# Kernel tuning notes

Hardware: AMD Instinct MI355X
Metric: run time of the kernel (lower is better)

The kernel has to match this reference:

```python
import jax, jax.numpy as jnp
import numpy as np

EPS_BN = 1e-5
EPS_W = 1e-8


def setup_inputs() -> dict:
    key = jax.random.key(0)
    ks = jax.random.split(key, 6)
    B, N, S, D1, D2 = 8, 8192, 2048, 128, 256
    Cin = D1 + D2  # 384
    return {
        "points_position": jax.random.normal(ks[0], (B, 3, N), jnp.float32),
        "sampled_points_position": jax.random.normal(ks[1], (B, 3, S), jnp.float32),
        "skip_points_feature": jax.random.normal(ks[2], (B, D1, N), jnp.float32),
        "sampled_points_feature": jax.random.normal(ks[3], (B, D2, S), jnp.float32),
        "W1": jax.random.normal(ks[4], (256, Cin), jnp.float32) * 0.05,
        "b1": jnp.zeros((256,), jnp.float32),
        "g1": jnp.ones((256,), jnp.float32),
        "beta1": jnp.zeros((256,), jnp.float32),
        "W2": jax.random.normal(ks[5], (128, 256), jnp.float32) * 0.05,
        "b2": jnp.zeros((128,), jnp.float32),
        "g2": jnp.ones((128,), jnp.float32),
        "beta2": jnp.zeros((128,), jnp.float32),
    }


def _bn_relu(x, g, b):
    # train-mode BatchNorm1d over (batch, points) per channel, x: [B,N,C]
    mean = jnp.mean(x, axis=(0, 1), keepdims=True)
    var = jnp.mean(jnp.square(x - mean), axis=(0, 1), keepdims=True)  # biased var
    return jax.nn.relu((x - mean) * jax.lax.rsqrt(var + EPS_BN) * g + b)


def reference(points_position, sampled_points_position, skip_points_feature,
              sampled_points_feature, W1, b1, g1, beta1, W2, b2, g2, beta2):
    pos = points_position.transpose(0, 2, 1)            # [B,N,3]
    spos = sampled_points_position.transpose(0, 2, 1)   # [B,S,3]
    sfeat = sampled_points_feature.transpose(0, 2, 1)   # [B,S,D2]

    # squared pairwise distance [B,N,S]
    d = (jnp.sum(pos * pos, axis=-1, keepdims=True)
         - 2.0 * jnp.einsum("bnc,bsc->bns", pos, spos)
         + jnp.sum(spos * spos, axis=-1)[:, None, :])

    # 3 nearest neighbors (smallest distances)
    neg_d3, idx = jax.lax.top_k(-d, 3)                  # [B,N,3]
    d3 = -neg_d3
    w = 1.0 / (d3 + EPS_W)
    w = w / jnp.sum(w, axis=-1, keepdims=True)          # [B,N,3]

    gathered = jax.vmap(lambda f, i: f[i])(sfeat, idx)  # [B,N,3,D2]
    interp = jnp.einsum("bnk,bnkd->bnd", w, gathered)   # [B,N,D2]

    feat = jnp.concatenate([skip_points_feature.transpose(0, 2, 1), interp], axis=-1)  # [B,N,D1+D2]

    h = _bn_relu(jnp.einsum("bnc,oc->bno", feat, W1) + b1, g1, beta1)  # [B,N,256]
    h = _bn_relu(jnp.einsum("bnc,oc->bno", h, W2) + b2, g2, beta2)     # [B,N,128]
    return h.transpose(0, 2, 1)                          # [B,128,N]
```

## Files before the change

### kernel.cpp

```cpp
#include <hip/hip_runtime.h>

constexpr int BATCH = 8;
constexpr int NPT   = 8192;
constexpr int NSMP  = 2048;
constexpr int D1C   = 128;
constexpr int D2C   = 256;
constexpr int CIN   = 384;
constexpr int C1    = 256;
constexpr int C2    = 128;
constexpr int BN_TOTAL = BATCH * NPT;

constexpr int WM = 128, WN = 64, WK = 32;
constexpr int NRB = BN_TOTAL / WM;

typedef __bf16 bf16x8 __attribute__((ext_vector_type(8)));
typedef short  s16x8  __attribute__((ext_vector_type(8)));
typedef float  f32x4  __attribute__((ext_vector_type(4)));

__device__ __forceinline__ unsigned short f2bf(float x) {
  unsigned u = __builtin_bit_cast(unsigned, x);
  u += 0x7fffu + ((u >> 16) & 1u);
  return (unsigned short)(u >> 16);
}
__device__ __forceinline__ float bf2f(unsigned short h) {
  return __builtin_bit_cast(float, (unsigned)h << 16);
}

__device__ __forceinline__ void gld_lds16(const void* g, void* l) {
  __builtin_amdgcn_global_load_lds(
      (const __attribute__((address_space(1))) void*)g,
      (__attribute__((address_space(3))) void*)l, 16, 0, 0);
}

__global__ void transpose_k(const float* __restrict__ in, float* __restrict__ out,
                            int rows, int cols, long inBatch, long outBatch) {
  __shared__ float tile[32][33];
  const float* inb = in + (size_t)blockIdx.z * inBatch;
  float* outb = out + (size_t)blockIdx.z * outBatch;
  int c0 = blockIdx.x * 32;
  int r0 = blockIdx.y * 32;
  int tx = threadIdx.x, ty = threadIdx.y;
#pragma unroll
  for (int i = 0; i < 32; i += 8) {
    int r = r0 + ty + i;
    tile[ty + i][tx] = inb[(size_t)r * cols + c0 + tx];
  }
  __syncthreads();
#pragma unroll
  for (int i = 0; i < 32; i += 8) {
    int c = c0 + ty + i;
    outb[(size_t)c * rows + r0 + tx] = tile[tx][ty + i];
  }
}

__global__ void skip_to_featB(const float* __restrict__ skip,
                              unsigned short* __restrict__ featB) {
  __shared__ float tile[32][33];
  int b = blockIdx.z;
  int n0 = blockIdx.x * 32;
  int d0 = blockIdx.y * 32;
  int tx = threadIdx.x, ty = threadIdx.y;
#pragma unroll
  for (int i = 0; i < 32; i += 8) {
    tile[ty + i][tx] = skip[((size_t)b * D1C + d0 + ty + i) * NPT + n0 + tx];
  }
  __syncthreads();
#pragma unroll
  for (int i = 0; i < 32; i += 8) {
    int n = n0 + ty + i;
    featB[((size_t)b * NPT + n) * CIN + d0 + tx] = f2bf(tile[tx][ty + i]);
  }
}

__global__ void wprep(const float* __restrict__ W, unsigned short* __restrict__ Wh,
                      int total) {
  int i = blockIdx.x * 256 + threadIdx.x;
  if (i >= total) return;
  Wh[i] = f2bf(W[i]);
}

__global__ void pack_spos(const float* __restrict__ spos, float* __restrict__ sposI) {
  int g = blockIdx.x * 256 + threadIdx.x;
  int b = g >> 11, s = g & (NSMP - 1);
  const float* sp = spos + (size_t)b * 3 * NSMP;
  sposI[(size_t)g * 3 + 0] = sp[s];
  sposI[(size_t)g * 3 + 1] = sp[NSMP + s];
  sposI[(size_t)g * 3 + 2] = sp[2 * NSMP + s];
}

constexpr int SEG = NSMP / 4;

__global__ __launch_bounds__(256) void knn_kernel(
    const float* __restrict__ pos,
    const float* __restrict__ sposI,
    int* __restrict__ idx_out,
    float* __restrict__ wgt_out,
    int* __restrict__ flag_list,
    int* __restrict__ flag_count) {
  __shared__ float qs[3 * NSMP];
  __shared__ float mk[4][4][64];

  int tid = threadIdx.x;
  int wave = tid >> 6, lane = tid & 63;
  int blk = blockIdx.x;
  int b = blk >> 7;
  int n = ((blk & 127) << 6) + lane;

  const float4* src = (const float4*)(sposI + (size_t)b * 3 * NSMP);
  float4* dst = (float4*)qs;
  for (int t = tid; t < 3 * NSMP / 4; t += 256) dst[t] = src[t];
  __syncthreads();

  const float* pb = pos + (size_t)b * 3 * NPT;
  float px = pb[n], py = pb[NPT + n], pz = pb[2 * NPT + n];

  const float INF = __builtin_inff();
  float k0 = INF, k1 = INF, k2 = INF, k3 = INF;

  const float4* q4 = (const float4*)qs;
  int s0 = wave * SEG;

#define KNN_STEP(QX, QY, QZ, SS)                                          \
  {                                                                       \
    float dx = px - (QX), dy = py - (QY), dz = pz - (QZ);                 \
    float d = fmaf(dx, dx, fmaf(dy, dy, dz * dz));                        \
    unsigned ki = (__builtin_bit_cast(unsigned, d) & 0xFFFFF800u) |       \
                  (unsigned)(SS);                                         \
    float kf = __builtin_bit_cast(float, ki);                             \
    float v1 = fmaxf(kf, k0); k0 = fminf(kf, k0);                         \
    float v2 = fmaxf(v1, k1); k1 = fminf(v1, k1);                         \
    float v3 = fmaxf(v2, k2); k2 = fminf(v2, k2);                         \
    k3 = fminf(v3, k3);                                                   \
  }

  for (int t = 0; t < SEG; t += 4) {
    int s = s0 + t;
    int u = 3 * (s >> 2);
    float4 qa = q4[u], qb = q4[u + 1], qc = q4[u + 2];
    KNN_STEP(qa.x, qa.y, qa.z, s + 0)
    KNN_STEP(qa.w, qb.x, qb.y, s + 1)
    KNN_STEP(qb.z, qb.w, qc.x, s + 2)
    KNN_STEP(qc.y, qc.z, qc.w, s + 3)
  }
#undef KNN_STEP

  mk[wave][0][lane] = k0; mk[wave][1][lane] = k1;
  mk[wave][2][lane] = k2; mk[wave][3][lane] = k3;
  __syncthreads();

  if (tid < 64) {
    float K0 = INF, K1 = INF, K2 = INF, K3 = INF;
#pragma unroll
    for (int w = 0; w < 4; w++) {
#pragma unroll
      for (int sl = 0; sl < 4; sl++) {
        float kf = mk[w][sl][tid];
        float v1 = fmaxf(kf, K0); K0 = fminf(kf, K0);
        float v2 = fmaxf(v1, K1); K1 = fminf(v1, K1);
        float v3 = fmaxf(v2, K2); K2 = fminf(v2, K2);
        K3 = fminf(v3, K3);
      }
    }
    int p = blk * 64 + tid;
    int I0 = (int)(__builtin_bit_cast(unsigned, K0) & 0x7FFu);
    int I1 = (int)(__builtin_bit_cast(unsigned, K1) & 0x7FFu);
    int I2 = (int)(__builtin_bit_cast(unsigned, K2) & 0x7FFu);
    float d2m = __builtin_bit_cast(float, __builtin_bit_cast(unsigned, K2) & 0xFFFFF800u);
    float d3m = __builtin_bit_cast(float, __builtin_bit_cast(unsigned, K3) & 0xFFFFF800u);
    bool flag = (d3m - d2m) < 2e-3f * d3m + 1e-7f;
    if (flag) {
      int slot = atomicAdd(flag_count, 1);
      flag_list[slot] = p;
    }
    const float* q = sposI + (size_t)b * 3 * NSMP;
    double pxd = (double)px, pyd = (double)py, pzd = (double)pz;
    double dd[3]; int II[3] = {I0, I1, I2};
#pragma unroll
    for (int k = 0; k < 3; k++) {
      double dx = pxd - (double)q[3 * II[k]];
      double dy = pyd - (double)q[3 * II[k] + 1];
      double dz = pzd - (double)q[3 * II[k] + 2];
      dd[k] = dx * dx + dy * dy + dz * dz;
    }
    double w0 = 1.0 / (dd[0] + 1e-8);
    double w1 = 1.0 / (dd[1] + 1e-8);
    double w2 = 1.0 / (dd[2] + 1e-8);
    double inv = 1.0 / (w0 + w1 + w2);
    size_t o = (size_t)p * 3;
    idx_out[o + 0] = I0; idx_out[o + 1] = I1; idx_out[o + 2] = I2;
    wgt_out[o + 0] = (float)(w0 * inv);
    wgt_out[o + 1] = (float)(w1 * inv);
    wgt_out[o + 2] = (float)(w2 * inv);
  }
}

__device__ __forceinline__ bool dless(double d, int i, double D, int I) {
  return d < D || (d == D && i < I);
}
__device__ __forceinline__ void dins3(double d, int i,
                                      double& b0, double& b1, double& b2,
                                      int& i0, int& i1, int& i2) {
  if (dless(d, i, b2, i2)) {
    if (dless(d, i, b1, i1)) {
      b2 = b1; i2 = i1;
      if (dless(d, i, b0, i0)) { b1 = b0; i1 = i0; b0 = d; i0 = i; }
      else                     { b1 = d; i1 = i; }
    } else { b2 = d; i2 = i; }
  }
}

__global__ __launch_bounds__(256) void knn_fallback(
    const float* __restrict__ pos, const float* __restrict__ sposI,
    const int* __restrict__ flag_list, const int* __restrict__ flag_count,
    int* __restrict__ idx_out, float* __restrict__ wgt_out) {
  int wave = threadIdx.x >> 6, lane = threadIdx.x & 63;
  int gw = blockIdx.x * 4 + wave;
  int cnt = *flag_count;
  for (int t = gw; t < cnt; t += 1024) {
    int p = flag_list[t];
    int b = p >> 13, n = p & (NPT - 1);
    const float* pb = pos + (size_t)b * 3 * NPT;
    double px = (double)pb[n], py = (double)pb[NPT + n], pz = (double)pb[2 * NPT + n];
    const float* q = sposI + (size_t)b * 3 * NSMP;
    double b0 = 1e300, b1 = 1e300, b2 = 1e300;
    int i0 = 0x7FFFFFFF, i1 = 0x7FFFFFFF, i2 = 0x7FFFFFFF;
    for (int s = lane; s < NSMP; s += 64) {
      double dx = px - (double)q[3 * s];
      double dy = py - (double)q[3 * s + 1];
      double dz = pz - (double)q[3 * s + 2];
      double d = dx * dx + dy * dy + dz * dz;
      dins3(d, s, b0, b1, b2, i0, i1, i2);
    }
#pragma unroll
    for (int m = 1; m < 64; m <<= 1) {
      double o0 = __shfl_xor(b0, m, 64), o1 = __shfl_xor(b1, m, 64), o2 = __shfl_xor(b2, m, 64);
      int    j0 = __shfl_xor(i0, m, 64), j1 = __shfl_xor(i1, m, 64), j2 = __shfl_xor(i2, m, 64);
      dins3(o0, j0, b0, b1, b2, i0, i1, i2);
      dins3(o1, j1, b0, b1, b2, i0, i1, i2);
      dins3(o2, j2, b0, b1, b2, i0, i1, i2);
    }
    if (lane == 0) {
      double w0 = 1.0 / (b0 + 1e-8);
      double w1 = 1.0 / (b1 + 1e-8);
      double w2 = 1.0 / (b2 + 1e-8);
      double inv = 1.0 / (w0 + w1 + w2);
      size_t o = (size_t)p * 3;
      idx_out[o + 0] = i0; idx_out[o + 1] = i1; idx_out[o + 2] = i2;
      wgt_out[o + 0] = (float)(w0 * inv);
      wgt_out[o + 1] = (float)(w1 * inv);
      wgt_out[o + 2] = (float)(w2 * inv);
    }
  }
}

__global__ __launch_bounds__(256) void interp_kernel(
    const float* __restrict__ sfeatT,
    const int* __restrict__ idx,
    const float* __restrict__ wgt,
    unsigned short* __restrict__ featB) {
  int p = blockIdx.x;
  int c = threadIdx.x;
  int b = p >> 13;
  size_t o = (size_t)p * 3;
  int i0 = idx[o], i1 = idx[o + 1], i2 = idx[o + 2];
  float w0 = wgt[o], w1 = wgt[o + 1], w2 = wgt[o + 2];
  const float* base = sfeatT + (size_t)b * NSMP * D2C;
  float v = w0 * base[(size_t)i0 * D2C + c]
          + w1 * base[(size_t)i1 * D2C + c]
          + w2 * base[(size_t)i2 * D2C + c];
  featB[(size_t)p * CIN + D1C + c] = f2bf(v);
}

__global__ __launch_bounds__(64) void gemm1_wave(
    const unsigned short* __restrict__ featB,
    const unsigned short* __restrict__ W1h,
    const float* __restrict__ bias,
    unsigned short* __restrict__ Y1,
    float* __restrict__ part_s,
    float* __restrict__ part_q) {
  __shared__ __align__(16) unsigned short As[WM * WK];
  __shared__ __align__(16) unsigned short Bs[WN * WK];
  int lane = threadIdx.x;
  int m16 = lane & 15, quad = lane >> 4;
  int rb = blockIdx.x, cb = blockIdx.y;
  int row0 = rb * WM, col0 = cb * WN;
  int row16 = lane >> 2, col8 = (lane & 3) * 8;

  f32x4 acc[8][4];
#pragma unroll
  for (int j = 0; j < 4; j++) {
    float bj = bias[col0 + j * 16 + m16];
#pragma unroll
    for (int i = 0; i < 8; i++) acc[i][j] = f32x4{bj, bj, bj, bj};
  }

  for (int k0 = 0; k0 < CIN; k0 += WK) {
#pragma unroll
    for (int c = 0; c < 8; c++)
      gld_lds16(&featB[(size_t)(row0 + c * 16 + row16) * CIN + k0 + col8],
                &As[c * 16 * WK]);
#pragma unroll
    for (int c = 0; c < 4; c++)
      gld_lds16(&W1h[(size_t)(col0 + c * 16 + row16) * CIN + k0 + col8],
                &Bs[c * 16 * WK]);
    __syncthreads();

    bf16x8 a[8], bf[4];
#pragma unroll
    for (int i = 0; i < 8; i++)
      a[i] = __builtin_bit_cast(bf16x8, *(const s16x8*)&As[(i * 16 + m16) * WK + quad * 8]);
#pragma unroll
    for (int j = 0; j < 4; j++)
      bf[j] = __builtin_bit_cast(bf16x8, *(const s16x8*)&Bs[(j * 16 + m16) * WK + quad * 8]);
#pragma unroll
    for (int i = 0; i < 8; i++)
#pragma unroll
      for (int j = 0; j < 4; j++)
        acc[i][j] = __builtin_amdgcn_mfma_f32_16x16x32_bf16(a[i], bf[j], acc[i][j], 0, 0, 0);
    __syncthreads();
  }

#pragma unroll
  for (int j = 0; j < 4; j++) {
    int col = col0 + j * 16 + m16;
    float s = 0.f, q = 0.f;
#pragma unroll
    for (int i = 0; i < 8; i++)
#pragma unroll
      for (int r = 0; r < 4; r++) {
        float v = acc[i][j][r];
        Y1[(size_t)(row0 + i * 16 + quad * 4 + r) * C1 + col] = f2bf(v);
        s += v; q = fmaf(v, v, q);
      }
    s += __shfl_xor(s, 16, 64); s += __shfl_xor(s, 32, 64);
    q += __shfl_xor(q, 16, 64); q += __shfl_xor(q, 32, 64);
    if (quad == 0) {
      part_s[(size_t)col * NRB + rb] = s;
      part_q[(size_t)col * NRB + rb] = q;
    }
  }
}

__global__ __launch_bounds__(64) void gemm2_wave(
    const unsigned short* __restrict__ Y1,
    const float* __restrict__ scale1, const float* __restrict__ shift1,
    const unsigned short* __restrict__ W2h,
    const float* __restrict__ bias,
    unsigned short* __restrict__ Y2,
    float* __restrict__ part_s,
    float* __restrict__ part_q) {
  __shared__ __align__(16) unsigned short As[WM * WK];
  __shared__ __align__(16) unsigned short Bs[WN * WK];
  __shared__ float scs[C1], shs[C1];
  int lane = threadIdx.x;
  int m16 = lane & 15, quad = lane >> 4;
  int rb = blockIdx.x, cb = blockIdx.y;
  int row0 = rb * WM, col0 = cb * WN;
  int row16 = lane >> 2, col8 = (lane & 3) * 8;

  for (int t = lane; t < C1; t += 64) { scs[t] = scale1[t]; shs[t] = shift1[t]; }

  f32x4 acc[8][4];
#pragma unroll
  for (int j = 0; j < 4; j++) {
    float bj = bias[col0 + j * 16 + m16];
#pragma unroll
    for (int i = 0; i < 8; i++) acc[i][j] = f32x4{bj, bj, bj, bj};
  }
  __syncthreads();

  for (int k0 = 0; k0 < C1; k0 += WK) {
#pragma unroll
    for (int c = 0; c < 4; c++)
      gld_lds16(&W2h[(size_t)(col0 + c * 16 + row16) * C1 + k0 + col8],
                &Bs[c * 16 * WK]);
#pragma unroll
    for (int c = 0; c < 8; c++) {
      int row = c * 16 + row16;
      s16x8 v = *(const s16x8*)&Y1[(size_t)(row0 + row) * C1 + k0 + col8];
      unsigned short ov[8];
#pragma unroll
      for (int e = 0; e < 8; e++) {
        float x = bf2f((unsigned short)v[e]);
        float y = fmaxf(fmaf(x, scs[k0 + col8 + e], shs[k0 + col8 + e]), 0.f);
        ov[e] = f2bf(y);
      }
      *(s16x8*)&As[row * WK + col8] = *(const s16x8*)ov;
    }
    __syncthreads();

    bf16x8 a[8], bf[4];
#pragma unroll
    for (int i = 0; i < 8; i++)
      a[i] = __builtin_bit_cast(bf16x8, *(const s16x8*)&As[(i * 16 + m16) * WK + quad * 8]);
#pragma unroll
    for (int j = 0; j < 4; j++)
      bf[j] = __builtin_bit_cast(bf16x8, *(const s16x8*)&Bs[(j * 16 + m16) * WK + quad * 8]);
#pragma unroll
    for (int i = 0; i < 8; i++)
#pragma unroll
      for (int j = 0; j < 4; j++)
        acc[i][j] = __builtin_amdgcn_mfma_f32_16x16x32_bf16(a[i], bf[j], acc[i][j], 0, 0, 0);
    __syncthreads();
  }

#pragma unroll
  for (int j = 0; j < 4; j++) {
    int col = col0 + j * 16 + m16;
    float s = 0.f, q = 0.f;
#pragma unroll
    for (int i = 0; i < 8; i++)
#pragma unroll
      for (int r = 0; r < 4; r++) {
        float v = acc[i][j][r];
        Y2[(size_t)(row0 + i * 16 + quad * 4 + r) * C2 + col] = f2bf(v);
        s += v; q = fmaf(v, v, q);
      }
    s += __shfl_xor(s, 16, 64); s += __shfl_xor(s, 32, 64);
    q += __shfl_xor(q, 16, 64); q += __shfl_xor(q, 32, 64);
    if (quad == 0) {
      part_s[(size_t)col * NRB + rb] = s;
      part_q[(size_t)col * NRB + rb] = q;
    }
  }
}

__global__ __launch_bounds__(256) void bn_reduce_coef(
    const float* __restrict__ part_s, const float* __restrict__ part_q, int nrb,
    const float* __restrict__ g, const float* __restrict__ beta,
    float* __restrict__ scale, float* __restrict__ shift) {
  int ch = blockIdx.x;
  int tid = threadIdx.x;
  float s = 0.f, q = 0.f;
  for (int t = tid; t < nrb; t += 256) {
    s += part_s[(size_t)ch * nrb + t];
    q += part_q[(size_t)ch * nrb + t];
  }
#pragma unroll
  for (int m = 1; m < 64; m <<= 1) {
    s += __shfl_xor(s, m, 64);
    q += __shfl_xor(q, m, 64);
  }
  __shared__ float ls[4], lq[4];
  int wave = tid >> 6;
  if ((tid & 63) == 0) { ls[wave] = s; lq[wave] = q; }
  __syncthreads();
  if (tid == 0) {
    s = ls[0] + ls[1] + ls[2] + ls[3];
    q = lq[0] + lq[1] + lq[2] + lq[3];
    const float invBN = 1.0f / (float)BN_TOTAL;
    float mean = s * invBN;
    float var = q * invBN - mean * mean;
    float sc = g[ch] / sqrtf(var + 1e-5f);
    scale[ch] = sc;
    shift[ch] = beta[ch] - mean * sc;
  }
}

__global__ void final_kernel(const unsigned short* __restrict__ Y2,
                             const float* __restrict__ scale, const float* __restrict__ shift,
                             float* __restrict__ out) {
  __shared__ float tile[32][33];
  int b = blockIdx.z;
  int n0 = blockIdx.x * 32;
  int c0 = blockIdx.y * 32;
  int tx = threadIdx.x, ty = threadIdx.y;
  float sc = scale[c0 + tx];
  float sh = shift[c0 + tx];
#pragma unroll
  for (int i = 0; i < 32; i += 8) {
    int n = n0 + ty + i;
    float v = bf2f(Y2[((size_t)b * NPT + n) * C2 + c0 + tx]);
    tile[ty + i][tx] = fmaxf(fmaf(v, sc, sh), 0.f);
  }
  __syncthreads();
#pragma unroll
  for (int i = 0; i < 32; i += 8) {
    int c = c0 + ty + i;
    out[((size_t)b * C2 + c) * NPT + n0 + tx] = tile[tx][ty + i];
  }
}

extern "C" void kernel_launch(void* const* d_in, const int* in_sizes, int n_in,
                              void* d_out, int out_size, void* d_ws, size_t ws_size,
                              hipStream_t stream) {
  (void)in_sizes; (void)n_in; (void)out_size; (void)ws_size;
  const float* pos   = (const float*)d_in[0];
  const float* spos  = (const float*)d_in[1];
  const float* skip  = (const float*)d_in[2];
  const float* sfeat = (const float*)d_in[3];
  const float* W1    = (const float*)d_in[4];
  const float* b1    = (const float*)d_in[5];
  const float* g1    = (const float*)d_in[6];
  const float* beta1 = (const float*)d_in[7];
  const float* W2    = (const float*)d_in[8];
  const float* b2    = (const float*)d_in[9];
  const float* g2    = (const float*)d_in[10];
  const float* beta2 = (const float*)d_in[11];
  float* out = (float*)d_out;

  float* ws = (float*)d_ws;
  size_t off = 0;
  float* sfeatT  = ws + off; off += (size_t)BATCH * NSMP * D2C;
  unsigned short* featB = (unsigned short*)(ws + off); off += (size_t)BN_TOTAL * CIN / 2;
  unsigned short* Y1    = (unsigned short*)(ws + off); off += (size_t)BN_TOTAL * C1 / 2;
  unsigned short* Y2    = (unsigned short*)(ws + off); off += (size_t)BN_TOTAL * C2 / 2;
  unsigned short* W1h   = (unsigned short*)(ws + off); off += (size_t)C1 * CIN / 2;
  unsigned short* W2h   = (unsigned short*)(ws + off); off += (size_t)C2 * C1 / 2;
  int*   knn_idx = (int*)(ws + off); off += (size_t)BN_TOTAL * 3;
  float* knn_w   = ws + off; off += (size_t)BN_TOTAL * 3;
  float* sposI   = ws + off; off += (size_t)BATCH * NSMP * 3;
  int* flag_list = (int*)(ws + off); off += (size_t)BN_TOTAL;
  float* part1_s = ws + off; off += (size_t)C1 * NRB;
  float* part1_q = ws + off; off += (size_t)C1 * NRB;
  float* part2_s = ws + off; off += (size_t)C2 * NRB;
  float* part2_q = ws + off; off += (size_t)C2 * NRB;
  float* stats   = ws + off; off += 2048;
  int*   flag_count = (int*)stats;
  float* scale1 = stats + 256, *shift1 = stats + 512;
  float* scale2 = stats + 768, *shift2 = stats + 1024;

  hipMemsetAsync(flag_count, 0, sizeof(int), stream);

  dim3 tb(32, 8);
  transpose_k<<<dim3(NSMP / 32, D2C / 32, BATCH), tb, 0, stream>>>(
      sfeat, sfeatT, D2C, NSMP, (long)D2C * NSMP, (long)NSMP * D2C);
  wprep<<<(C1 * CIN + 255) / 256, 256, 0, stream>>>(W1, W1h, C1 * CIN);
  wprep<<<(C2 * C1 + 255) / 256, 256, 0, stream>>>(W2, W2h, C2 * C1);
  skip_to_featB<<<dim3(NPT / 32, D1C / 32, BATCH), tb, 0, stream>>>(skip, featB);

  pack_spos<<<BATCH * NSMP / 256, 256, 0, stream>>>(spos, sposI);
  knn_kernel<<<BN_TOTAL / 64, 256, 0, stream>>>(pos, sposI, knn_idx, knn_w,
                                                flag_list, flag_count);
  knn_fallback<<<256, 256, 0, stream>>>(pos, sposI, flag_list, flag_count,
                                        knn_idx, knn_w);
  interp_kernel<<<BN_TOTAL, 256, 0, stream>>>(sfeatT, knn_idx, knn_w, featB);

  gemm1_wave<<<dim3(NRB, C1 / WN), 64, 0, stream>>>(
      featB, W1h, b1, Y1, part1_s, part1_q);
  bn_reduce_coef<<<C1, 256, 0, stream>>>(part1_s, part1_q, NRB, g1, beta1, scale1, shift1);

  gemm2_wave<<<dim3(NRB, C2 / WN), 64, 0, stream>>>(
      Y1, scale1, shift1, W2h, b2, Y2, part2_s, part2_q);
  bn_reduce_coef<<<C2, 256, 0, stream>>>(part2_s, part2_q, NRB, g2, beta2, scale2, shift2);

  final_kernel<<<dim3(NPT / 32, C2 / 32, BATCH), tb, 0, stream>>>(Y2, scale2, shift2, out);
}
```

Before: 315.6 us.

## Expand KNN distance into dot-product form and use med3 top-4 insertion

Precomputes -2*q and |q|^2 per sampled point in a float4 layout so each candidate distance takes three FMAs instead of subtracts plus squares. Replaces the min/max insertion network with fmed3-based insertion to cut VALU ops in the inner KNN loop. The expanded form loses precision through cancellation, so the near-tie flag threshold is loosened, which can send more points to the fallback path. Shared memory per block grows from 24KB to 32KB.

```diff
diff --git a/kernel.cpp b/kernel.cpp
--- a/kernel.cpp
+++ b/kernel.cpp
@@ -79,25 +79,39 @@
   Wh[i] = f2bf(W[i]);
 }
 
-__global__ void pack_spos(const float* __restrict__ spos, float* __restrict__ sposI) {
+__global__ void pack_spos(const float* __restrict__ spos, float* __restrict__ sposI,
+                          float4* __restrict__ qs4) {
   int g = blockIdx.x * 256 + threadIdx.x;
   int b = g >> 11, s = g & (NSMP - 1);
   const float* sp = spos + (size_t)b * 3 * NSMP;
-  sposI[(size_t)g * 3 + 0] = sp[s];
-  sposI[(size_t)g * 3 + 1] = sp[NSMP + s];
-  sposI[(size_t)g * 3 + 2] = sp[2 * NSMP + s];
+  float x = sp[s], y = sp[NSMP + s], z = sp[2 * NSMP + s];
+  sposI[(size_t)g * 3 + 0] = x;
+  sposI[(size_t)g * 3 + 1] = y;
+  sposI[(size_t)g * 3 + 2] = z;
+  qs4[g] = make_float4(-2.f * x, -2.f * y, -2.f * z,
+                       fmaf(x, x, fmaf(y, y, z * z)));
 }
 
 constexpr int SEG = NSMP / 4;
+
+__device__ __forceinline__ void ins_med3(float kf, float& k0, float& k1,
+                                         float& k2, float& k3) {
+  float o0 = k0, o1 = k1, o2 = k2;
+  k0 = fminf(kf, o0);
+  k1 = __builtin_amdgcn_fmed3f(kf, o0, o1);
+  k2 = __builtin_amdgcn_fmed3f(kf, o1, o2);
+  k3 = __builtin_amdgcn_fmed3f(kf, o2, k3);
+}
 
 __global__ __launch_bounds__(256) void knn_kernel(
     const float* __restrict__ pos,
+    const float4* __restrict__ qs4g,
     const float* __restrict__ sposI,
     int* __restrict__ idx_out,
     float* __restrict__ wgt_out,
     int* __restrict__ flag_list,
     int* __restrict__ flag_count) {
-  __shared__ float qs[3 * NSMP];
+  __shared__ float4 qs[NSMP];
   __shared__ float mk[4][4][64];
 
   int tid = threadIdx.x;
@@ -106,41 +120,34 @@
   int b = blk >> 7;
   int n = ((blk & 127) << 6) + lane;
 
-  const float4* src = (const float4*)(sposI + (size_t)b * 3 * NSMP);
-  float4* dst = (float4*)qs;
-  for (int t = tid; t < 3 * NSMP / 4; t += 256) dst[t] = src[t];
+  const float4* src = qs4g + (size_t)b * NSMP;
+  for (int t = tid; t < NSMP; t += 256) qs[t] = src[t];
   __syncthreads();
 
   const float* pb = pos + (size_t)b * 3 * NPT;
   float px = pb[n], py = pb[NPT + n], pz = pb[2 * NPT + n];
+  float pp = fmaf(px, px, fmaf(py, py, pz * pz));
 
   const float INF = __builtin_inff();
   float k0 = INF, k1 = INF, k2 = INF, k3 = INF;
 
-  const float4* q4 = (const float4*)qs;
   int s0 = wave * SEG;
 
-#define KNN_STEP(QX, QY, QZ, SS)                                          \
+#define KNN_STEP(Q, SS)                                                   \
   {                                                                       \
-    float dx = px - (QX), dy = py - (QY), dz = pz - (QZ);                 \
-    float d = fmaf(dx, dx, fmaf(dy, dy, dz * dz));                        \
+    float d = fmaf(px, (Q).x, fmaf(py, (Q).y, fmaf(pz, (Q).z, (Q).w + pp))); \
     unsigned ki = (__builtin_bit_cast(unsigned, d) & 0xFFFFF800u) |       \
                   (unsigned)(SS);                                         \
-    float kf = __builtin_bit_cast(float, ki);                             \
-    float v1 = fmaxf(kf, k0); k0 = fminf(kf, k0);                         \
-    float v2 = fmaxf(v1, k1); k1 = fminf(v1, k1);                         \
-    float v3 = fmaxf(v2, k2); k2 = fminf(v2, k2);                         \
-    k3 = fminf(v3, k3);                                                   \
+    ins_med3(__builtin_bit_cast(float, ki), k0, k1, k2, k3);              \
   }
 
   for (int t = 0; t < SEG; t += 4) {
     int s = s0 + t;
-    int u = 3 * (s >> 2);
-    float4 qa = q4[u], qb = q4[u + 1], qc = q4[u + 2];
-    KNN_STEP(qa.x, qa.y, qa.z, s + 0)
-    KNN_STEP(qa.w, qb.x, qb.y, s + 1)
-    KNN_STEP(qb.z, qb.w, qc.x, s + 2)
-    KNN_STEP(qc.y, qc.z, qc.w, s + 3)
+    float4 qa = qs[s], qb = qs[s + 1], qc = qs[s + 2], qd = qs[s + 3];
+    KNN_STEP(qa, s + 0)
+    KNN_STEP(qb, s + 1)
+    KNN_STEP(qc, s + 2)
+    KNN_STEP(qd, s + 3)
   }
 #undef KNN_STEP
 
@@ -151,23 +158,18 @@
   if (tid < 64) {
     float K0 = INF, K1 = INF, K2 = INF, K3 = INF;
 #pragma unroll
-    for (int w = 0; w < 4; w++) {
-#pragma unroll
-      for (int sl = 0; sl < 4; sl++) {
-        float kf = mk[w][sl][tid];
-        float v1 = fmaxf(kf, K0); K0 = fminf(kf, K0);
-        float v2 = fmaxf(v1, K1); K1 = fminf(v1, K1);
-        float v3 = fmaxf(v2, K2); K2 = fminf(v2, K2);
-        K3 = fminf(v3, K3);
-      }
-    }
+    for (int w = 0; w < 4; w++)
+#pragma unroll
+      for (int sl = 0; sl < 4; sl++)
+        ins_med3(mk[w][sl][tid], K0, K1, K2, K3);
+
     int p = blk * 64 + tid;
     int I0 = (int)(__builtin_bit_cast(unsigned, K0) & 0x7FFu);
     int I1 = (int)(__builtin_bit_cast(unsigned, K1) & 0x7FFu);
     int I2 = (int)(__builtin_bit_cast(unsigned, K2) & 0x7FFu);
     float d2m = __builtin_bit_cast(float, __builtin_bit_cast(unsigned, K2) & 0xFFFFF800u);
     float d3m = __builtin_bit_cast(float, __builtin_bit_cast(unsigned, K3) & 0xFFFFF800u);
-    bool flag = (d3m - d2m) < 2e-3f * d3m + 1e-7f;
+    bool flag = (d3m - d2m) < 2e-3f * fmaxf(d3m, 0.f) + 1e-5f;
     if (flag) {
       int slot = atomicAdd(flag_count, 1);
       flag_list[slot] = p;
@@ -510,6 +512,7 @@
   int*   knn_idx = (int*)(ws + off); off += (size_t)BN_TOTAL * 3;
   float* knn_w   = ws + off; off += (size_t)BN_TOTAL * 3;
   float* sposI   = ws + off; off += (size_t)BATCH * NSMP * 3;
+  float4* qs4    = (float4*)(ws + off); off += (size_t)BATCH * NSMP * 4;
   int* flag_list = (int*)(ws + off); off += (size_t)BN_TOTAL;
   float* part1_s = ws + off; off += (size_t)C1 * NRB;
   float* part1_q = ws + off; off += (size_t)C1 * NRB;
@@ -529,8 +532,8 @@
   wprep<<<(C2 * C1 + 255) / 256, 256, 0, stream>>>(W2, W2h, C2 * C1);
   skip_to_featB<<<dim3(NPT / 32, D1C / 32, BATCH), tb, 0, stream>>>(skip, featB);
 
-  pack_spos<<<BATCH * NSMP / 256, 256, 0, stream>>>(spos, sposI);
-  knn_kernel<<<BN_TOTAL / 64, 256, 0, stream>>>(pos, sposI, knn_idx, knn_w,
+  pack_spos<<<BATCH * NSMP / 256, 256, 0, stream>>>(spos, sposI, qs4);
+  knn_kernel<<<BN_TOTAL / 64, 256, 0, stream>>>(pos, qs4, sposI, knn_idx, knn_w,
                                                 flag_list, flag_count);
   knn_fallback<<<256, 256, 0, stream>>>(pos, sposI, flag_list, flag_count,
                                         knn_idx, knn_w);
```

Result: faster. 301.7 us (-4.4%).
